# Optimization experiments

Measured on AMD Instinct MI355X. Metric: run time of the kernel, lower is better.

## Reference

```python
import jax, jax.numpy as jnp
import numpy as np

IMG_H, IMG_W = 448, 800
GRID = 224
MIN_SIZE = 64.0
B, N, NCAM = 1, 48, 6


def setup_inputs() -> dict:
    rng = np.random.default_rng(0)
    centers = np.stack([rng.uniform(-40, 40, (B, N)), rng.uniform(-40, 40, (B, N)),
                        rng.uniform(-1.5, 0.5, (B, N))], -1)
    dims = rng.uniform(1.0, 4.0, (B, N, 3))
    heading = rng.uniform(-np.pi, np.pi, (B, N, 1))
    boxes7 = np.concatenate([centers, dims, heading], -1).astype(np.float32)
    gt_labels = rng.integers(1, 11, (B, N)).astype(np.int64)  # 1..10 as in gt_boxes[...,-1]
    imgs = rng.random((B, NCAM, 3, IMG_H, IMG_W)).astype(np.float32)
    # plausible lidar->image projections: 6 outward-facing cams, 60 deg apart, 90 deg hfov
    fx = fy = 400.0
    K = np.array([[fx, 0, IMG_W / 2], [0, fy, IMG_H / 2], [0, 0, 1]], np.float32)
    l2i = np.zeros((B, NCAM, 4, 4), np.float32)
    for c in range(NCAM):
        th = 2 * np.pi * c / NCAM
        right = np.array([np.sin(th), -np.cos(th), 0.0])
        down = np.array([0.0, 0.0, -1.0])
        fwdv = np.array([np.cos(th), np.sin(th), 0.0])
        R = np.stack([right, down, fwdv])  # lidar -> cam
        l2i[:, c, :3, :3] = K @ R
        l2i[:, c, 3, 3] = 1.0
    eye4 = np.eye(4, dtype=np.float32)
    img_aug = np.broadcast_to(eye4, (B, NCAM, 4, 4)).copy()
    lidar_aug = np.broadcast_to(eye4, (B, 4, 4)).copy()
    W_img = (rng.standard_normal((588, 768)) * 0.02).astype(np.float32)
    text_features = rng.standard_normal((10, 768)).astype(np.float32)
    return dict(boxes7=jnp.asarray(boxes7), gt_labels=jnp.asarray(gt_labels),
                camera_imgs=jnp.asarray(imgs), lidar2image=jnp.asarray(l2i),
                img_aug_matrix=jnp.asarray(img_aug), lidar_aug_matrix=jnp.asarray(lidar_aug),
                W_img=jnp.asarray(W_img), text_features=jnp.asarray(text_features),
                logit_scale=jnp.asarray(np.float32(np.log(100.0))))


def _boxes_to_corners_3d(boxes7):  # (M,7) -> (M,8,3)
    template = jnp.array([[1, 1, -1], [1, -1, -1], [-1, -1, -1], [-1, 1, -1],
                          [1, 1, 1], [1, -1, 1], [-1, -1, 1], [-1, 1, 1]], jnp.float32) * 0.5
    corners = boxes7[:, None, 3:6] * template[None]
    c, s = jnp.cos(boxes7[:, 6]), jnp.sin(boxes7[:, 6])
    z, o = jnp.zeros_like(c), jnp.ones_like(c)
    rot = jnp.stack([c, s, z, -s, c, z, z, z, o], -1).reshape(-1, 3, 3)
    corners = jnp.einsum('nki,nij->nkj', corners, rot)  # points @ R as in torch code
    return corners + boxes7[:, None, :3]


def _project(corners, l2i, img_aug, lidar_aug):
    # corners (M,3); l2i/img_aug (6,4,4); lidar_aug (4,4)
    pts = corners - lidar_aug[:3, 3]
    pts = jnp.linalg.inv(lidar_aug[:3, :3]) @ pts.T  # (3,M)
    p = jnp.einsum('cij,jm->cim', l2i[:, :3, :3], pts) + l2i[:, :3, 3][:, :, None]
    zc = jnp.clip(p[:, 2], 1e-5, 1e5)
    xy = p[:, :2] / zc[:, None]
    p = jnp.concatenate([xy, zc[:, None]], axis=1)  # (6,3,M)
    p = jnp.einsum('cij,cjm->cim', img_aug[:, :3, :3], p) + img_aug[:, :3, 3][:, :, None]
    rc = p[:, :2].transpose(0, 2, 1)[..., ::-1]  # (6,M,2) as (row, col)
    on_img = (rc[..., 0] < IMG_H) & (rc[..., 0] >= 0) & (rc[..., 1] < IMG_W) & (rc[..., 1] >= 0)
    return rc, on_img


def _bilinear(img, ix, iy):
    # img (3,H,W); ix, iy (N,GRID,GRID) pixel coords; zero padding, align_corners=False
    x0f, y0f = jnp.floor(ix), jnp.floor(iy)
    wx1, wy1 = ix - x0f, iy - y0f
    wx0, wy0 = 1.0 - wx1, 1.0 - wy1

    def gather(xf, yf):
        valid = (xf >= 0) & (xf <= IMG_W - 1) & (yf >= 0) & (yf <= IMG_H - 1)
        xi = jnp.clip(xf.astype(jnp.int32), 0, IMG_W - 1)
        yi = jnp.clip(yf.astype(jnp.int32), 0, IMG_H - 1)
        return img[:, yi, xi] * valid[None].astype(img.dtype)  # (3,N,G,G)

    return (gather(x0f, y0f) * (wx0 * wy0)[None] + gather(x0f + 1, y0f) * (wx1 * wy0)[None]
            + gather(x0f, y0f + 1) * (wx0 * wy1)[None] + gather(x0f + 1, y0f + 1) * (wx1 * wy1)[None])


def _forward(boxes7, gt_labels, camera_imgs, lidar2image, img_aug_matrix,
             lidar_aug_matrix, W_img, text_features, logit_scale):
    Bx, Nx = boxes7.shape[:2]
    corners = _boxes_to_corners_3d(boxes7.reshape(-1, 7)).reshape(Bx, Nx * 8, 3)
    rc, on_img = jax.vmap(_project)(corners, lidar2image, img_aug_matrix, lidar_aug_matrix)
    # .long() in torch truncates toward zero; coords are constants wrt grads
    all_coords = jax.lax.stop_gradient(jnp.trunc(rc)).astype(jnp.int32).reshape(Bx, NCAM, Nx, 8, 2)
    visible = on_img.reshape(Bx, NCAM, Nx, 8).any(-1)  # (B,6,N)
    rows, cols = all_coords[..., 0], all_coords[..., 1]
    x1 = jnp.clip(cols.min(-1), 0, IMG_W)
    x2 = jnp.clip(cols.max(-1), 0, IMG_W)
    y1 = jnp.clip(rows.min(-1), 0, IMG_H)
    y2 = jnp.clip(rows.max(-1), 0, IMG_H)
    sq = jnp.maximum(jnp.maximum(x2 - x1, y2 - y1).astype(jnp.float32), MIN_SIZE)
    u = jnp.linspace(0.0, 1.0, GRID)  # normalized affine_grid after min/max rescale
    px = x1.astype(jnp.float32)[..., None, None] + sq[..., None, None] * u[None, None, None, None, :]
    py = y1.astype(jnp.float32)[..., None, None] + sq[..., None, None] * u[None, None, None, :, None]
    gx = px / IMG_W * 2.0 - 1.0
    gy = py / IMG_H * 2.0 - 1.0
    ix = ((gx + 1.0) * IMG_W - 1.0) / 2.0  # unnormalize (align_corners=False)
    iy = ((gy + 1.0) * IMG_H - 1.0) / 2.0
    patches = jax.vmap(jax.vmap(_bilinear))(camera_imgs, ix, iy)  # (B,6,3,N,G,G)
    patches = patches.transpose(0, 1, 3, 2, 4, 5)  # (B,6,N,3,G,G)
    # stub CLIP image tower: 16x16 avg pool -> flatten -> linear to 768
    pooled = patches.reshape(Bx, NCAM, Nx, 3, 14, 16, 14, 16).mean(axis=(5, 7))
    feats = pooled.reshape(Bx, NCAM, Nx, 588) @ W_img  # (B,6,N,768)
    feats = feats / jnp.linalg.norm(feats, axis=-1, keepdims=True)
    text_n = text_features / jnp.linalg.norm(text_features, axis=-1, keepdims=True)
    logits = jnp.exp(logit_scale) * jnp.einsum('bcnd,kd->bcnk', feats, text_n)
    probs = jax.nn.softmax(logits, axis=-1) * visible[..., None].astype(logits.dtype)
    cnt = visible.sum(1).astype(probs.dtype)  # (B,N) cameras per box
    mean_probs = probs.sum(1) / jnp.maximum(cnt, 1.0)[..., None]  # (B,N,10)
    pred = jnp.argmax(mean_probs, axis=-1).reshape(-1)
    true = gt_labels.reshape(-1) - 1
    acc = (pred == true).astype(jnp.float32).mean()
    return pred, true, acc, mean_probs


def reference(boxes7, gt_labels, camera_imgs, lidar2image, img_aug_matrix,
              lidar_aug_matrix, W_img, text_features, logit_scale):
    return _forward(boxes7, gt_labels, camera_imgs, lidar2image, img_aug_matrix,
                    lidar_aug_matrix, W_img, text_features, logit_scale)
```

## Files before the change

kernel.cpp:

```cpp
#include <hip/hip_runtime.h>
#include <math.h>

#define IMG_H 448
#define IMG_W 800
#define GRIDN 224
#define NCAM 6
#define NBOX 48
#define NPAIR (NCAM * NBOX)
#define NCLASS 10
#define FEATD 768
#define POOLD 588
#define PROWS 14
#define KSPLIT 4
#define KCH 147

#define WS_PAIR 0
#define WS_POOL (NPAIR * 4)
#define WS_FEAT (WS_POOL + NPAIR * POOLD)
#define WS_PROBS (WS_FEAT + NPAIR * KSPLIT * FEATD)

__global__ void __launch_bounds__(256) pool_kernel(const float* __restrict__ imgs,
                                                   const float* __restrict__ boxes7,
                                                   const float* __restrict__ l2i,
                                                   const float* __restrict__ img_aug,
                                                   const float* __restrict__ lidar_aug,
                                                   float* __restrict__ ws) {
    int pair = blockIdx.x / PROWS;
    int pr = blockIdx.x % PROWS;
    int cam = pair / NBOX, box = pair % NBOX;
    int tid = threadIdx.x;

    __shared__ float s_pw[4];

    if (tid < 8) {
        int k = tid;
        float R[9];
        for (int i = 0; i < 3; ++i)
            for (int j = 0; j < 3; ++j) R[i * 3 + j] = lidar_aug[i * 4 + j];
        float ltx = lidar_aug[3], lty = lidar_aug[7], ltz = lidar_aug[11];
        float det = R[0] * (R[4] * R[8] - R[5] * R[7]) - R[1] * (R[3] * R[8] - R[5] * R[6]) +
                    R[2] * (R[3] * R[7] - R[4] * R[6]);
        float i0 = (R[4] * R[8] - R[5] * R[7]) / det;
        float i1 = (R[2] * R[7] - R[1] * R[8]) / det;
        float i2 = (R[1] * R[5] - R[2] * R[4]) / det;
        float i3 = (R[5] * R[6] - R[3] * R[8]) / det;
        float i4 = (R[0] * R[8] - R[2] * R[6]) / det;
        float i5 = (R[2] * R[3] - R[0] * R[5]) / det;
        float i6 = (R[3] * R[7] - R[4] * R[6]) / det;
        float i7 = (R[1] * R[6] - R[0] * R[7]) / det;
        float i8 = (R[0] * R[4] - R[1] * R[3]) / det;

        const float* M = l2i + cam * 16;
        const float* A = img_aug + cam * 16;
        const float* bxp = boxes7 + box * 7;
        float cx = bxp[0], cy = bxp[1], cz = bxp[2];
        float dx = bxp[3], dy = bxp[4], dz = bxp[5], hd = bxp[6];
        float ch = cosf(hd), sh = sinf(hd);
        float tx = (k & 2) ? -0.5f : 0.5f;
        float ty = ((k + 1) & 2) ? -0.5f : 0.5f;
        float tz = (k & 4) ? 0.5f : -0.5f;
        float lx = dx * tx, ly = dy * ty, lz = dz * tz;
        float wx = lx * ch - ly * sh + cx;
        float wy = lx * sh + ly * ch + cy;
        float wz = lz + cz;
        float px_ = wx - ltx, py_ = wy - lty, pz_ = wz - ltz;
        float qx = i0 * px_ + i1 * py_ + i2 * pz_;
        float qy = i3 * px_ + i4 * py_ + i5 * pz_;
        float qz = i6 * px_ + i7 * py_ + i8 * pz_;
        float p0 = M[0] * qx + M[1] * qy + M[2] * qz + M[3];
        float p1 = M[4] * qx + M[5] * qy + M[6] * qz + M[7];
        float p2 = M[8] * qx + M[9] * qy + M[10] * qz + M[11];
        float zc = fminf(fmaxf(p2, 1e-5f), 1e5f);
        float sx = p0 / zc, sy = p1 / zc;
        float q0 = A[0] * sx + A[1] * sy + A[2] * zc + A[3];
        float q1 = A[4] * sx + A[5] * sy + A[6] * zc + A[7];
        float row = q1, col = q0;
        int on = (row < (float)IMG_H) && (row >= 0.f) && (col < (float)IMG_W) && (col >= 0.f);
        int ri = (int)row;
        int ci = (int)col;
        int minr = ri, maxr = ri, minc = ci, maxc = ci, visv = on;
        for (int off = 4; off >= 1; off >>= 1) {
            minr = min(minr, __shfl_xor(minr, off, 8));
            maxr = max(maxr, __shfl_xor(maxr, off, 8));
            minc = min(minc, __shfl_xor(minc, off, 8));
            maxc = max(maxc, __shfl_xor(maxc, off, 8));
            visv |= __shfl_xor(visv, off, 8);
        }
        if (tid == 0) {
            int x1 = min(max(minc, 0), IMG_W);
            int x2 = min(max(maxc, 0), IMG_W);
            int y1 = min(max(minr, 0), IMG_H);
            int y2 = min(max(maxr, 0), IMG_H);
            float sq = fmaxf((float)max(x2 - x1, y2 - y1), 64.0f);
            s_pw[0] = (float)x1;
            s_pw[1] = (float)y1;
            s_pw[2] = sq;
            s_pw[3] = visv ? 1.0f : 0.0f;
            if (pr == 0) {
                float* pw = ws + WS_PAIR + pair * 4;
                pw[0] = (float)x1; pw[1] = (float)y1; pw[2] = sq;
                pw[3] = visv ? 1.0f : 0.0f;
            }
        }
    }
    __syncthreads();
    if (s_pw[3] == 0.f) return;
    float bx1 = s_pw[0], by1 = s_pw[1], sq = s_pw[2];

    const float* img0 = imgs + (size_t)cam * 3 * IMG_H * IMG_W;
    const float* img1 = img0 + (size_t)(IMG_H * IMG_W);
    const float* img2 = img0 + (size_t)(2 * IMG_H * IMG_W);
    bool active = tid < GRIDN;

    const float ustep = 1.0f / 223.0f;
    float wx0 = 0.f, wx1 = 0.f, mx0 = 0.f, mx1 = 0.f;
    int xi0 = 0, xi1 = 0;
    if (active) {
        float u = (float)tid * ustep;
        float px = bx1 + sq * u;
        float gx = px / (float)IMG_W * 2.0f - 1.0f;
        float ix = ((gx + 1.0f) * (float)IMG_W - 1.0f) / 2.0f;
        float x0f = floorf(ix);
        wx1 = ix - x0f;
        wx0 = 1.0f - wx1;
        float x1f = x0f + 1.0f;
        mx0 = (x0f >= 0.f && x0f <= (float)(IMG_W - 1)) ? 1.f : 0.f;
        mx1 = (x1f >= 0.f && x1f <= (float)(IMG_W - 1)) ? 1.f : 0.f;
        xi0 = min(max((int)x0f, 0), IMG_W - 1);
        xi1 = min(max((int)x1f, 0), IMG_W - 1);
    }

    int iyA = -0x40000000, iyB = -0x40000000;
    float vA00 = 0.f, vA01 = 0.f, vA10 = 0.f, vA11 = 0.f, vA20 = 0.f, vA21 = 0.f;
    float vB00 = 0.f, vB01 = 0.f, vB10 = 0.f, vB11 = 0.f, vB20 = 0.f, vB21 = 0.f;

    float acc0 = 0.f, acc1 = 0.f, acc2 = 0.f;
    for (int r = 0; r < 16; ++r) {
        int i = pr * 16 + r;
        float u = (float)i * ustep;
        float py = by1 + sq * u;
        float gy = py / (float)IMG_H * 2.0f - 1.0f;
        float iy = ((gy + 1.0f) * (float)IMG_H - 1.0f) / 2.0f;
        float y0f = floorf(iy);
        float wy1 = iy - y0f;
        float wy0 = 1.0f - wy1;
        float y1f = y0f + 1.0f;
        float my0 = (y0f >= 0.f && y0f <= (float)(IMG_H - 1)) ? 1.f : 0.f;
        float my1 = (y1f >= 0.f && y1f <= (float)(IMG_H - 1)) ? 1.f : 0.f;
        int yi0 = min(max((int)y0f, 0), IMG_H - 1);
        int yi1 = min(max((int)y1f, 0), IMG_H - 1);
        if (yi0 != iyA || yi1 != iyB) {
            if (yi0 == iyB) {
                vA00 = vB00; vA01 = vB01; vA10 = vB10; vA11 = vB11; vA20 = vB20; vA21 = vB21;
                iyA = iyB;
            } else if (yi0 != iyA) {
                if (active) {
                    int r0 = yi0 * IMG_W;
                    vA00 = img0[r0 + xi0]; vA01 = img0[r0 + xi1];
                    vA10 = img1[r0 + xi0]; vA11 = img1[r0 + xi1];
                    vA20 = img2[r0 + xi0]; vA21 = img2[r0 + xi1];
                }
                iyA = yi0;
            }
            if (yi1 != iyB) {
                if (active) {
                    int r1 = yi1 * IMG_W;
                    vB00 = img0[r1 + xi0]; vB01 = img0[r1 + xi1];
                    vB10 = img1[r1 + xi0]; vB11 = img1[r1 + xi1];
                    vB20 = img2[r1 + xi0]; vB21 = img2[r1 + xi1];
                }
                iyB = yi1;
            }
        }
        if (active) {
            float w00 = wx0 * wy0, w10 = wx1 * wy0, w01 = wx0 * wy1, w11 = wx1 * wy1;
            float m00 = mx0 * my0, m10 = mx1 * my0, m01 = mx0 * my1, m11 = mx1 * my1;
            acc0 += vA00 * m00 * w00 + vA01 * m10 * w10 + vB00 * m01 * w01 + vB01 * m11 * w11;
            acc1 += vA10 * m00 * w00 + vA11 * m10 * w10 + vB10 * m01 * w01 + vB11 * m11 * w11;
            acc2 += vA20 * m00 * w00 + vA21 * m10 * w10 + vB20 * m01 * w01 + vB21 * m11 * w11;
        }
    }
    for (int off = 8; off >= 1; off >>= 1) {
        acc0 += __shfl_xor(acc0, off, 16);
        acc1 += __shfl_xor(acc1, off, 16);
        acc2 += __shfl_xor(acc2, off, 16);
    }
    if (active && (tid & 15) == 0) {
        int pj = tid >> 4;
        float* pool = ws + WS_POOL + (size_t)pair * POOLD;
        pool[0 * 196 + pr * 14 + pj] = acc0 * (1.0f / 256.0f);
        pool[1 * 196 + pr * 14 + pj] = acc1 * (1.0f / 256.0f);
        pool[2 * 196 + pr * 14 + pj] = acc2 * (1.0f / 256.0f);
    }
}

__global__ void __launch_bounds__(768) head1_kernel(const float* __restrict__ W,
                                                    float* __restrict__ ws) {
    int pair = blockIdx.x / KSPLIT;
    int kc = blockIdx.x % KSPLIT;
    if (ws[WS_PAIR + pair * 4 + 3] == 0.f) return;
    int tid = threadIdx.x;
    __shared__ float pk[KCH];
    if (tid < KCH) pk[tid] = ws[WS_POOL + (size_t)pair * POOLD + kc * KCH + tid];
    __syncthreads();
    const float* Wp = W + (size_t)(kc * KCH) * FEATD + tid;
    float f = 0.f;
#pragma unroll 7
    for (int k = 0; k < KCH; ++k) f += pk[k] * Wp[(size_t)k * FEATD];
    ws[WS_FEAT + ((size_t)pair * KSPLIT + kc) * FEATD + tid] = f;
}

__global__ void __launch_bounds__(256) head2_kernel(const float* __restrict__ text,
                                                    const float* __restrict__ ls_ptr,
                                                    float* __restrict__ ws) {
    int pair = blockIdx.x;
    int tid = threadIdx.x;
    const float* pw = ws + WS_PAIR + pair * 4;
    if (pw[3] == 0.f) {
        if (tid < NCLASS) ws[WS_PROBS + pair * NCLASS + tid] = 0.f;
        return;
    }
    const float* fb = ws + WS_FEAT + (size_t)pair * KSPLIT * FEATD;
    float f0 = 0.f, f1 = 0.f, f2 = 0.f;
    for (int kc = 0; kc < KSPLIT; ++kc) {
        const float* fp = fb + (size_t)kc * FEATD;
        f0 += fp[tid];
        f1 += fp[tid + 256];
        f2 += fp[tid + 512];
    }
    float pn = f0 * f0 + f1 * f1 + f2 * f2;
    float pl[NCLASS], tq[NCLASS];
    for (int k = 0; k < NCLASS; ++k) {
        const float* tr = text + (size_t)k * FEATD;
        float t0 = tr[tid], t1 = tr[tid + 256], t2 = tr[tid + 512];
        pl[k] = f0 * t0 + f1 * t1 + f2 * t2;
        tq[k] = t0 * t0 + t1 * t1 + t2 * t2;
    }
    for (int off = 32; off >= 1; off >>= 1) {
        pn += __shfl_xor(pn, off);
        for (int k = 0; k < NCLASS; ++k) {
            pl[k] += __shfl_xor(pl[k], off);
            tq[k] += __shfl_xor(tq[k], off);
        }
    }
    __shared__ float rn[4];
    __shared__ float rl[4][NCLASS];
    __shared__ float rq[4][NCLASS];
    int wave = tid >> 6, lane = tid & 63;
    if (lane == 0) {
        rn[wave] = pn;
        for (int k = 0; k < NCLASS; ++k) { rl[wave][k] = pl[k]; rq[wave][k] = tq[k]; }
    }
    __syncthreads();
    if (tid == 0) {
        float n2 = rn[0] + rn[1] + rn[2] + rn[3];
        float nrm = sqrtf(n2);
        float scale = expf(ls_ptr[0]);
        float lg[NCLASS], m = -1e30f;
        for (int k = 0; k < NCLASS; ++k) {
            float d = rl[0][k] + rl[1][k] + rl[2][k] + rl[3][k];
            float tn = sqrtf(rq[0][k] + rq[1][k] + rq[2][k] + rq[3][k]);
            lg[k] = scale * (d / (nrm * tn));
            m = fmaxf(m, lg[k]);
        }
        float s = 0.f;
        for (int k = 0; k < NCLASS; ++k) {
            lg[k] = expf(lg[k] - m);
            s += lg[k];
        }
        float* probs = ws + WS_PROBS + pair * NCLASS;
        for (int k = 0; k < NCLASS; ++k) probs[k] = lg[k] / s;
    }
}

__global__ void finalize_kernel(const int* __restrict__ gt, const float* __restrict__ ws,
                                float* __restrict__ out) {
    int n = threadIdx.x;
    bool match = false;
    if (n < NBOX) {
        const float* probs = ws + WS_PROBS;
        float cnt = 0.f;
        for (int c = 0; c < NCAM; ++c)
            cnt += (ws[WS_PAIR + (c * NBOX + n) * 4 + 3] != 0.f) ? 1.f : 0.f;
        float denom = fmaxf(cnt, 1.0f);
        float mp[NCLASS];
        for (int k = 0; k < NCLASS; ++k) {
            float s = 0.f;
            for (int c = 0; c < NCAM; ++c) s += probs[(c * NBOX + n) * NCLASS + k];
            mp[k] = s / denom;
            out[97 + n * NCLASS + k] = mp[k];
        }
        float best = mp[0];
        int pred = 0;
        for (int k = 1; k < NCLASS; ++k)
            if (mp[k] > best) { best = mp[k]; pred = k; }
        int tr = gt[n] - 1;
        out[n] = (float)pred;
        out[NBOX + n] = (float)tr;
        match = (pred == tr);
    }
    unsigned long long b = __ballot(match);
    if (n == 0) out[2 * NBOX] = (float)__popcll(b) / (float)NBOX;
}

extern "C" void kernel_launch(void* const* d_in, const int* in_sizes, int n_in,
                              void* d_out, int out_size, void* d_ws, size_t ws_size,
                              hipStream_t stream) {
    const float* boxes7 = (const float*)d_in[0];
    const int* gt = (const int*)d_in[1];
    const float* imgs = (const float*)d_in[2];
    const float* l2i = (const float*)d_in[3];
    const float* img_aug = (const float*)d_in[4];
    const float* lidar_aug = (const float*)d_in[5];
    const float* W = (const float*)d_in[6];
    const float* text = (const float*)d_in[7];
    const float* ls = (const float*)d_in[8];
    float* ws = (float*)d_ws;
    float* out = (float*)d_out;

    pool_kernel<<<NPAIR * PROWS, 256, 0, stream>>>(imgs, boxes7, l2i, img_aug, lidar_aug, ws);
    head1_kernel<<<NPAIR * KSPLIT, 768, 0, stream>>>(W, ws);
    head2_kernel<<<NPAIR, 256, 0, stream>>>(text, ls, ws);
    finalize_kernel<<<1, 64, 0, stream>>>(gt, ws, out);
}
```

Measured before the change: 48.73 us.

## Fuse pooling with partial GEMV per row block and drop head1 kernel

Each pool block now keeps its 42 pooled values in shared memory and multiplies them straight against the matching 42 rows of W. It writes a 768-wide partial feature per (pair, row) instead of writing pooled values to the workspace. The separate head1 GEMV launch and the pooled round trip through global memory go away, and the head reduction now sums 14 partials instead of 4. In exchange, partial-sum traffic grows. Blocks for invisible pairs may also do GEMV work that head1 used to skip.

```diff
diff --git a/kernel.cpp b/kernel.cpp
--- a/kernel.cpp
+++ b/kernel.cpp
@@ -11,26 +11,25 @@
 #define FEATD 768
 #define POOLD 588
 #define PROWS 14
-#define KSPLIT 4
-#define KCH 147
 
 #define WS_PAIR 0
-#define WS_POOL (NPAIR * 4)
-#define WS_FEAT (WS_POOL + NPAIR * POOLD)
-#define WS_PROBS (WS_FEAT + NPAIR * KSPLIT * FEATD)
-
-__global__ void __launch_bounds__(256) pool_kernel(const float* __restrict__ imgs,
-                                                   const float* __restrict__ boxes7,
-                                                   const float* __restrict__ l2i,
-                                                   const float* __restrict__ img_aug,
-                                                   const float* __restrict__ lidar_aug,
-                                                   float* __restrict__ ws) {
+#define WS_PART (NPAIR * 4)
+#define WS_PROBS (WS_PART + NPAIR * PROWS * FEATD)
+
+__global__ void __launch_bounds__(256) pool_gemv_kernel(const float* __restrict__ imgs,
+                                                        const float* __restrict__ boxes7,
+                                                        const float* __restrict__ l2i,
+                                                        const float* __restrict__ img_aug,
+                                                        const float* __restrict__ lidar_aug,
+                                                        const float* __restrict__ W,
+                                                        float* __restrict__ ws) {
     int pair = blockIdx.x / PROWS;
     int pr = blockIdx.x % PROWS;
     int cam = pair / NBOX, box = pair % NBOX;
     int tid = threadIdx.x;
 
     __shared__ float s_pw[4];
+    __shared__ float s_pool[3 * 14];
 
     if (tid < 8) {
         int k = tid;
@@ -187,32 +186,34 @@
     }
     if (active && (tid & 15) == 0) {
         int pj = tid >> 4;
-        float* pool = ws + WS_POOL + (size_t)pair * POOLD;
-        pool[0 * 196 + pr * 14 + pj] = acc0 * (1.0f / 256.0f);
-        pool[1 * 196 + pr * 14 + pj] = acc1 * (1.0f / 256.0f);
-        pool[2 * 196 + pr * 14 + pj] = acc2 * (1.0f / 256.0f);
-    }
+        s_pool[0 * 14 + pj] = acc0 * (1.0f / 256.0f);
+        s_pool[1 * 14 + pj] = acc1 * (1.0f / 256.0f);
+        s_pool[2 * 14 + pj] = acc2 * (1.0f / 256.0f);
+    }
+    __syncthreads();
+
+    float f0 = 0.f, f1 = 0.f, f2 = 0.f;
+#pragma unroll
+    for (int c = 0; c < 3; ++c) {
+        const float* Wc = W + ((size_t)(c * 196 + pr * 14)) * FEATD;
+#pragma unroll 14
+        for (int pj = 0; pj < 14; ++pj) {
+            float p = s_pool[c * 14 + pj];
+            const float* wr = Wc + (size_t)pj * FEATD;
+            f0 += p * wr[tid];
+            f1 += p * wr[tid + 256];
+            f2 += p * wr[tid + 512];
+        }
+    }
+    float* po = ws + WS_PART + ((size_t)pair * PROWS + pr) * FEATD;
+    po[tid] = f0;
+    po[tid + 256] = f1;
+    po[tid + 512] = f2;
 }
 
-__global__ void __launch_bounds__(768) head1_kernel(const float* __restrict__ W,
-                                                    float* __restrict__ ws) {
-    int pair = blockIdx.x / KSPLIT;
-    int kc = blockIdx.x % KSPLIT;
-    if (ws[WS_PAIR + pair * 4 + 3] == 0.f) return;
-    int tid = threadIdx.x;
-    __shared__ float pk[KCH];
-    if (tid < KCH) pk[tid] = ws[WS_POOL + (size_t)pair * POOLD + kc * KCH + tid];
-    __syncthreads();
-    const float* Wp = W + (size_t)(kc * KCH) * FEATD + tid;
-    float f = 0.f;
-#pragma unroll 7
-    for (int k = 0; k < KCH; ++k) f += pk[k] * Wp[(size_t)k * FEATD];
-    ws[WS_FEAT + ((size_t)pair * KSPLIT + kc) * FEATD + tid] = f;
-}
-
-__global__ void __launch_bounds__(256) head2_kernel(const float* __restrict__ text,
-                                                    const float* __restrict__ ls_ptr,
-                                                    float* __restrict__ ws) {
+__global__ void __launch_bounds__(256) headred_kernel(const float* __restrict__ text,
+                                                      const float* __restrict__ ls_ptr,
+                                                      float* __restrict__ ws) {
     int pair = blockIdx.x;
     int tid = threadIdx.x;
     const float* pw = ws + WS_PAIR + pair * 4;
@@ -220,10 +221,10 @@
         if (tid < NCLASS) ws[WS_PROBS + pair * NCLASS + tid] = 0.f;
         return;
     }
-    const float* fb = ws + WS_FEAT + (size_t)pair * KSPLIT * FEATD;
+    const float* pb = ws + WS_PART + (size_t)pair * PROWS * FEATD;
     float f0 = 0.f, f1 = 0.f, f2 = 0.f;
-    for (int kc = 0; kc < KSPLIT; ++kc) {
-        const float* fp = fb + (size_t)kc * FEATD;
+    for (int pr = 0; pr < PROWS; ++pr) {
+        const float* fp = pb + (size_t)pr * FEATD;
         f0 += fp[tid];
         f1 += fp[tid + 256];
         f2 += fp[tid + 512];
@@ -318,8 +319,8 @@
     float* ws = (float*)d_ws;
     float* out = (float*)d_out;
 
-    pool_kernel<<<NPAIR * PROWS, 256, 0, stream>>>(imgs, boxes7, l2i, img_aug, lidar_aug, ws);
-    head1_kernel<<<NPAIR * KSPLIT, 768, 0, stream>>>(W, ws);
-    head2_kernel<<<NPAIR, 256, 0, stream>>>(text, ls, ws);
+    pool_gemv_kernel<<<NPAIR * PROWS, 256, 0, stream>>>(imgs, boxes7, l2i, img_aug,
+                                                        lidar_aug, W, ws);
+    headred_kernel<<<NPAIR, 256, 0, stream>>>(text, ls, ws);
     finalize_kernel<<<1, 64, 0, stream>>>(gt, ws, out);
 }
```

Result: faster. 44.11 us (-9.5%).
